# Kernel tuning notes

Measured on AMD Instinct MI355X. Metric: run time of the kernel, lower is better.

Reference implementation:

```python
import jax, jax.numpy as jnp
import numpy as np

N = 1_000_000   # total nodes
B = 20_000      # number of graphs (segments)
V = 100_000     # item vocab (rows of feat table)
D = 128         # input_dim
H = 128         # hidden_dim
O = 256         # output_dim
EPS = 1e-5


def setup_inputs() -> dict:
    key = jax.random.key(0)
    ks = jax.random.split(key, 10)
    feat = jax.random.normal(ks[0], (V, D), dtype=jnp.float32)
    iid = jax.random.randint(ks[1], (N,), 0, V)
    segment_ids = jnp.sort(jax.random.randint(ks[2], (N,), 0, B))
    last_nodes = jax.random.randint(ks[3], (B,), 0, N)
    s = 1.0 / np.sqrt(D)
    gamma = jnp.ones((D,), jnp.float32)
    beta = jnp.zeros((D,), jnp.float32)
    W_u = jax.random.uniform(ks[4], (D, H), jnp.float32, -s, s)
    W_v = jax.random.uniform(ks[5], (D, H), jnp.float32, -s, s)
    b_v = jax.random.uniform(ks[6], (H,), jnp.float32, -s, s)
    w_e = jax.random.uniform(ks[7], (H,), jnp.float32, -1.0 / np.sqrt(H), 1.0 / np.sqrt(H))
    W_out = jax.random.uniform(ks[8], (D, O), jnp.float32, -s, s)
    return {"feat": feat, "iid": iid, "segment_ids": segment_ids,
            "last_nodes": last_nodes, "gamma": gamma, "beta": beta,
            "W_u": W_u, "W_v": W_v, "b_v": b_v, "w_e": w_e, "W_out": W_out}


def reference(feat, iid, segment_ids, last_nodes, gamma, beta, W_u, W_v, b_v, w_e, W_out):
    # gather per-node features from item table
    x = feat[iid]                                  # [N, D]
    # BatchNorm1d (training mode: batch statistics, biased var)
    mean = jnp.mean(x, axis=0)
    var = jnp.mean((x - mean) ** 2, axis=0)
    x = (x - mean) * jax.lax.rsqrt(var + EPS) * gamma + beta
    # projections
    feat_u = x @ W_u                               # [N, H]
    feat_v = x[last_nodes] @ W_v + b_v             # [B, H]
    e = jax.nn.sigmoid(feat_u + feat_v[segment_ids]) @ w_e   # [N]
    # segment softmax over per-graph node segments
    e_max = jax.ops.segment_max(e, segment_ids, num_segments=B)
    ex = jnp.exp(e - e_max[segment_ids])
    denom = jax.ops.segment_sum(ex, segment_ids, num_segments=B)
    alpha = ex / denom[segment_ids]                # [N]
    # weighted segment sum, then output projection
    rst = jax.ops.segment_sum(x * alpha[:, None], segment_ids, num_segments=B)  # [B, D]
    return rst @ W_out                             # [B, O]
```

## Files before the change

### kernel.cpp

```cpp
#include <hip/hip_runtime.h>

typedef __attribute__((ext_vector_type(8))) short short8;
typedef __attribute__((ext_vector_type(4))) float floatx4;

static __device__ __forceinline__ unsigned short f2bf(float x) {
    unsigned int u = __float_as_uint(x);
    u += 0x7fffu + ((u >> 16) & 1u);
    return (unsigned short)(u >> 16);
}

__global__ void k_hist(const int* __restrict__ iid, int* __restrict__ counts, int N) {
    int n = blockIdx.x * blockDim.x + threadIdx.x;
    if (n < N) atomicAdd(&counts[iid[n]], 1);
}

__global__ __launch_bounds__(256) void k_cvtstats(const float* __restrict__ feat,
                                                  const int* __restrict__ counts,
                                                  unsigned short* __restrict__ featb,
                                                  float* __restrict__ dsum, float* __restrict__ dsumsq,
                                                  int V) {
    int tid = threadIdx.x;
    int r2 = tid >> 7, d = tid & 127;
    float s = 0.f, qa = 0.f;
    for (int vp = blockIdx.x; vp * 2 < V; vp += gridDim.x) {
        int v = vp * 2 + r2;
        if (v >= V) continue;
        float f = feat[(size_t)v * 128 + d];
        featb[(size_t)v * 128 + d] = f2bf(f);
        float c = (float)counts[v];
        if (c != 0.f) { s += c * f; qa += c * f * f; }
    }
    __shared__ float red[256];
    red[tid] = s; __syncthreads();
    if (tid < 128) atomicAdd(&dsum[d], red[tid] + red[tid + 128]);
    __syncthreads();
    red[tid] = qa; __syncthreads();
    if (tid < 128) atomicAdd(&dsumsq[d], red[tid] + red[tid + 128]);
}

__global__ __launch_bounds__(128) void k_affine(const float* __restrict__ sum,
                                                const float* __restrict__ sumsq,
                                                const float* __restrict__ gamma,
                                                const float* __restrict__ beta,
                                                float* __restrict__ scale, float* __restrict__ shift,
                                                float invN) {
    int d = threadIdx.x;
    float mean = sum[d] * invN;
    float var  = sumsq[d] * invN - mean * mean;
    float sc   = gamma[d] * rsqrtf(var + 1e-5f);
    scale[d] = sc;
    shift[d] = beta[d] - mean * sc;
}

__global__ __launch_bounds__(128) void k_prep(const float* __restrict__ Wu, const float* __restrict__ Wv,
                                              const float* __restrict__ bv,
                                              const float* __restrict__ scale, const float* __restrict__ shift,
                                              unsigned short* __restrict__ wut, float* __restrict__ wvs,
                                              float* __restrict__ cbias) {
    int h = blockIdx.x, d = threadIdx.x;
    float sc = scale[d], sh = shift[d];
    float wu = Wu[d * 128 + h], wv = Wv[d * 128 + h];
    wut[h * 128 + d] = f2bf(sc * wu);
    wvs[d * 128 + h] = sc * wv;
    __shared__ float red[128];
    red[d] = sh * (wu + wv);
    __syncthreads();
    for (int off = 64; off > 0; off >>= 1) {
        if (d < off) red[d] += red[d + off];
        __syncthreads();
    }
    if (d == 0) cbias[h] = bv[h] + red[0];
}

__global__ __launch_bounds__(128) void k_fv(const float* __restrict__ feat, const int* __restrict__ iid,
                                            const int* __restrict__ last, const float* __restrict__ wvs,
                                            const float* __restrict__ cbias, float* __restrict__ fv,
                                            int B) {
    const int GPB = 8;
    int b0 = blockIdx.x * GPB;
    int h = threadIdx.x;
    __shared__ float sx[GPB][128];
    for (int g = 0; g < GPB; ++g) {
        int b = b0 + g;
        if (b < B) {
            int row = iid[last[b]];
            sx[g][h] = feat[(size_t)row * 128 + h];
        }
    }
    __syncthreads();
    float acc[GPB];
#pragma unroll
    for (int g = 0; g < GPB; ++g) acc[g] = 0.f;
    for (int d = 0; d < 128; ++d) {
        float w = wvs[d * 128 + h];
#pragma unroll
        for (int g = 0; g < GPB; ++g) acc[g] += sx[g][d] * w;
    }
    float c = cbias[h];
    for (int g = 0; g < GPB; ++g)
        if (b0 + g < B) fv[(size_t)(b0 + g) * 128 + h] = acc[g] + c;
}

__global__ __launch_bounds__(256, 3) void k_main(
        const unsigned short* __restrict__ featb, const int* __restrict__ iid,
        const int* __restrict__ seg, const unsigned short* __restrict__ wut,
        const float* __restrict__ fv, const float* __restrict__ we_g,
        float* __restrict__ exo, int N, int B, int numTiles) {
    __shared__ unsigned short sA[2][64 * 128];
    __shared__ int   sSeg[2][64];
    __shared__ float sFv[2][4][128];
    __shared__ float sEp[2][4][64];

    int tid = threadIdx.x;
    int wv = tid >> 6, lane = tid & 63, q = lane >> 4, c = lane & 15;
    int p2 = lane & 15;
    int rowbase = wv * 16 + (lane >> 4);

    short8 bfr[2][4];
    float we2[2];
#pragma unroll
    for (int t = 0; t < 2; ++t) {
        int h = (2 * wv + t) * 16 + c;
        we2[t] = we_g[h];
#pragma unroll
        for (int kc = 0; kc < 4; ++kc)
            bfr[t][kc] = *(const short8*)(wut + h * 128 + kc * 32 + q * 8);
    }

    if (blockIdx.x >= numTiles) return;

    int iidR[4]; int segR; float2 fvR;
    auto loadRegs = [&](int T) {
        int n0 = T << 6;
#pragma unroll
        for (int k = 0; k < 4; ++k)
            iidR[k] = iid[min(n0 + rowbase + 4 * k, N - 1)];
        segR = seg[min(n0 + (tid & 63), N - 1)];
        int s0 = seg[min(n0, N - 1)];
        int fvrow = min(s0 + (tid >> 6), B - 1);
        fvR = *(const float2*)(fv + (size_t)fvrow * 128 + ((tid << 1) & 127));
    };
    auto stage = [&](int buf) {
        unsigned short* sAb = &sA[buf][0];
#pragma unroll
        for (int k = 0; k < 4; ++k) {
            int row = rowbase + 4 * k;
            int j = (p2 & 8) | ((p2 & 7) ^ (row & 7));
            const unsigned short* g = featb + (size_t)iidR[k] * 128 + j * 8;
            __builtin_amdgcn_global_load_lds(
                (const __attribute__((address_space(1))) void*)g,
                (__attribute__((address_space(3))) void*)(sAb + wv * 2048 + k * 512),
                16, 0, 0);
        }
        if (tid < 64) sSeg[buf][tid] = segR;
        *(float2*)&sFv[buf][tid >> 6][(tid << 1) & 127] = fvR;
    };

    int T = blockIdx.x;
    loadRegs(T);
    stage(0);
    int prevN0 = -1;
    int cur = 0;

    for (;;) {
        int Tn = T + gridDim.x;
        bool hn = (Tn < numTiles);
        if (hn) loadRegs(Tn);
        __syncthreads();
        if (hn) stage(cur ^ 1);

        floatx4 acc[4][2];
#pragma unroll
        for (int mt = 0; mt < 4; ++mt)
#pragma unroll
            for (int t = 0; t < 2; ++t) acc[mt][t] = (floatx4)(0.f);
#pragma unroll
        for (int kc = 0; kc < 4; ++kc) {
            int jj = 4 * kc + q;
            int pofs = ((jj & 8) | ((jj & 7) ^ (c & 7))) * 8;
            short8 a0 = *(const short8*)&sA[cur][( 0 + c) * 128 + pofs];
            short8 a1 = *(const short8*)&sA[cur][(16 + c) * 128 + pofs];
            short8 a2 = *(const short8*)&sA[cur][(32 + c) * 128 + pofs];
            short8 a3 = *(const short8*)&sA[cur][(48 + c) * 128 + pofs];
#pragma unroll
            for (int t = 0; t < 2; ++t) {
                acc[0][t] = __builtin_amdgcn_mfma_f32_16x16x32_bf16(a0, bfr[t][kc], acc[0][t], 0, 0, 0);
                acc[1][t] = __builtin_amdgcn_mfma_f32_16x16x32_bf16(a1, bfr[t][kc], acc[1][t], 0, 0, 0);
                acc[2][t] = __builtin_amdgcn_mfma_f32_16x16x32_bf16(a2, bfr[t][kc], acc[2][t], 0, 0, 0);
                acc[3][t] = __builtin_amdgcn_mfma_f32_16x16x32_bf16(a3, bfr[t][kc], acc[3][t], 0, 0, 0);
            }
        }
        {
            int s0 = sSeg[cur][0];
            int h0 = wv * 32 + c;
#pragma unroll
            for (int mt = 0; mt < 4; ++mt)
#pragma unroll
                for (int r = 0; r < 4; ++r) {
                    int nl = mt * 16 + q * 4 + r;
                    int sg = sSeg[cur][nl];
                    int off = sg - s0;
                    float f0, f1;
                    if (off < 4) {
                        f0 = sFv[cur][off][h0];
                        f1 = sFv[cur][off][h0 + 16];
                    } else {
                        f0 = fv[((size_t)sg << 7) + h0];
                        f1 = fv[((size_t)sg << 7) + h0 + 16];
                    }
                    float u0 = acc[mt][0][r] + f0;
                    float u1 = acc[mt][1][r] + f1;
                    float p = we2[0] * __builtin_amdgcn_rcpf(1.f + __expf(-u0))
                            + we2[1] * __builtin_amdgcn_rcpf(1.f + __expf(-u1));
                    p += __shfl_xor(p, 1);
                    p += __shfl_xor(p, 2);
                    p += __shfl_xor(p, 4);
                    p += __shfl_xor(p, 8);
                    if (c == 0) sEp[cur][wv][nl] = p;
                }
        }
        if (prevN0 >= 0 && tid < 64) {
            int n = prevN0 + tid;
            if (n < N) {
                float s = sEp[cur ^ 1][0][tid] + sEp[cur ^ 1][1][tid]
                        + sEp[cur ^ 1][2][tid] + sEp[cur ^ 1][3][tid];
                exo[n] = __expf(s);
            }
        }
        prevN0 = T << 6;
        if (!hn) break;
        T = Tn; cur ^= 1;
    }
    __syncthreads();
    if (tid < 64) {
        int n = prevN0 + tid;
        if (n < N) {
            float s = sEp[cur][0][tid] + sEp[cur][1][tid]
                    + sEp[cur][2][tid] + sEp[cur][3][tid];
            exo[n] = __expf(s);
        }
    }
}

__global__ void k_bounds(const int* __restrict__ seg, int* __restrict__ start, int N, int B) {
    int n = blockIdx.x * blockDim.x + threadIdx.x;
    if (n >= N) return;
    int cur = seg[n];
    int prev = (n == 0) ? -1 : seg[n - 1];
    for (int b = prev + 1; b <= cur; ++b) start[b] = n;
    if (n == N - 1)
        for (int b = cur + 1; b <= B; ++b) start[b] = N;
}

__global__ __launch_bounds__(256) void k_wsum(const unsigned short* __restrict__ featb,
                                              const int* __restrict__ iid,
                                              const float* __restrict__ exv,
                                              const int* __restrict__ start,
                                              const float* __restrict__ scale,
                                              const float* __restrict__ shift,
                                              float* __restrict__ rst, int B) {
    int tid = threadIdx.x;
    int wv = tid >> 6, lane = tid & 63;
    int b = blockIdx.x * 4 + wv;
    if (b >= B) return;
    int s = start[b], t = start[b + 1];
    float a0 = 0.f, a1 = 0.f, dl = 0.f;
    int voff = lane * 2;

    for (int base = s; base < t; base += 64) {
        int idx = base + lane;
        bool valid = (idx < t);
        float e = valid ? exv[idx] : 0.f;
        int   r = valid ? iid[idx] : 0;
        dl += e;
        for (int k = 0; k < 64; k += 4) {
            if (base + k >= t) break;
#pragma unroll
            for (int kk = 0; kk < 4; ++kk) {
                int   rk = __builtin_amdgcn_readlane(r, k + kk);
                float ek = __int_as_float(__builtin_amdgcn_readlane(__float_as_int(e), k + kk));
                unsigned u = *(const unsigned*)(featb + (size_t)rk * 128 + voff);
                a0 += ek * __uint_as_float(u << 16);
                a1 += ek * __uint_as_float(u & 0xffff0000u);
            }
        }
    }
#pragma unroll
    for (int off = 1; off < 64; off <<= 1) dl += __shfl_xor(dl, off);
    float inv = (t > s) ? 1.f / dl : 0.f;
    float msk = (t > s) ? 1.f : 0.f;
    int d0 = lane * 2;
    float r0 = scale[d0] * a0 * inv + shift[d0] * msk;
    float r1 = scale[d0 + 1] * a1 * inv + shift[d0 + 1] * msk;
    *(float2*)&rst[((size_t)b << 7) + d0] = make_float2(r0, r1);
}

__global__ __launch_bounds__(256) void k_out(const float* __restrict__ rst, const float* __restrict__ Wout,
                                             float* __restrict__ out, int B) {
    __shared__ float sT[128][36];
    int b0 = blockIdx.x * 32;
    int t = threadIdx.x;
    for (int i = 0; i < 16; ++i) {
        int idx = i * 256 + t;
        int r = idx >> 7, d = idx & 127;
        int b = min(b0 + r, B - 1);
        sT[d][r] = rst[((size_t)b << 7) + d];
    }
    __syncthreads();
    float acc[32];
#pragma unroll
    for (int r = 0; r < 32; ++r) acc[r] = 0.f;
    for (int dd = 0; dd < 128; ++dd) {
        float w = Wout[dd * 256 + t];
        const float4* row = (const float4*)&sT[dd][0];
#pragma unroll
        for (int r4 = 0; r4 < 8; ++r4) {
            float4 v = row[r4];
            acc[r4 * 4 + 0] += w * v.x;
            acc[r4 * 4 + 1] += w * v.y;
            acc[r4 * 4 + 2] += w * v.z;
            acc[r4 * 4 + 3] += w * v.w;
        }
    }
    for (int r = 0; r < 32; ++r)
        if (b0 + r < B) out[(size_t)(b0 + r) * 256 + t] = acc[r];
}

extern "C" void kernel_launch(void* const* d_in, const int* in_sizes, int n_in,
                              void* d_out, int out_size, void* d_ws, size_t ws_size,
                              hipStream_t stream) {
    const float* feat  = (const float*)d_in[0];
    const int*   iid   = (const int*)d_in[1];
    const int*   seg   = (const int*)d_in[2];
    const int*   last  = (const int*)d_in[3];
    const float* gamma = (const float*)d_in[4];
    const float* beta  = (const float*)d_in[5];
    const float* Wu    = (const float*)d_in[6];
    const float* Wv    = (const float*)d_in[7];
    const float* bv    = (const float*)d_in[8];
    const float* we    = (const float*)d_in[9];
    const float* Wout  = (const float*)d_in[10];
    float* out = (float*)d_out;

    int V = in_sizes[0] / 128;
    int N = in_sizes[1];
    int B = in_sizes[3];

    char* w = (char*)d_ws;
    size_t off = 0;
    auto alloc = [&](size_t bytes) -> void* {
        void* p = w + off;
        off += (bytes + 255) & ~(size_t)255;
        return p;
    };
    int*   counts = (int*)alloc((size_t)V * 4);
    float* dsum   = (float*)alloc(512);
    float* dsumsq = (float*)alloc(512);
    size_t zero_bytes = off;
    float* scale  = (float*)alloc(512);
    float* shift  = (float*)alloc(512);
    float* cbias  = (float*)alloc(512);
    unsigned short* wut = (unsigned short*)alloc(128 * 128 * 2);
    float* wvs    = (float*)alloc(128 * 128 * 4);
    float* fv     = (float*)alloc((size_t)B * 128 * 4);
    unsigned short* featb = (unsigned short*)alloc((size_t)V * 128 * 2);
    float* exo    = (float*)alloc((size_t)N * 4);
    int*   startA = (int*)alloc((size_t)(B + 1) * 4);
    float* rst    = (float*)alloc((size_t)B * 128 * 4);
    (void)ws_size; (void)n_in; (void)out_size;

    hipMemsetAsync(d_ws, 0, zero_bytes, stream);

    k_hist<<<(N + 255) / 256, 256, 0, stream>>>(iid, counts, N);
    k_cvtstats<<<1024, 256, 0, stream>>>(feat, counts, featb, dsum, dsumsq, V);
    k_affine<<<1, 128, 0, stream>>>(dsum, dsumsq, gamma, beta, scale, shift, 1.0f / (float)N);
    k_prep<<<128, 128, 0, stream>>>(Wu, Wv, bv, scale, shift, wut, wvs, cbias);
    k_fv<<<(B + 7) / 8, 128, 0, stream>>>(feat, iid, last, wvs, cbias, fv, B);
    k_bounds<<<(N + 255) / 256, 256, 0, stream>>>(seg, startA, N, B);

    int numTiles = (N + 63) / 64;
    k_main<<<768, 256, 0, stream>>>(featb, iid, seg, wut, fv, we, exo, N, B, numTiles);

    k_wsum<<<(B + 3) / 4, 256, 0, stream>>>(featb, iid, exo, startA, scale, shift, rst, B);
    k_out<<<(B + 31) / 32, 256, 0, stream>>>(rst, Wout, out, B);
}
```

Baseline: 413.4 us.

## Fuse weighted segment sum into main kernel using staged LDS tiles and atomics

The main attention kernel now does the weighted segment accumulation itself. It reuses the bf16 feature tile already staged in LDS and pushes per-segment partial sums and denominators to global buffers with float atomics. This drops the exo write/readback, the k_bounds and k_wsum kernels, and the second gather of feature rows. Softmax normalisation and the BatchNorm affine are deferred into k_out. It also swaps the shuffle reduction for DPP adds, raises occupancy to 4 blocks with 1024 blocks, and adds a sync per tile. The exp no longer subtracts the segment max, which risks overflow, and atomics add contention plus nondeterminism.

New measurement: 413.8 us. About the same (+0.1%).

```diff
diff --git a/kernel.cpp b/kernel.cpp
--- a/kernel.cpp
+++ b/kernel.cpp
@@ -2,11 +2,18 @@
 
 typedef __attribute__((ext_vector_type(8))) short short8;
 typedef __attribute__((ext_vector_type(4))) float floatx4;
+typedef __attribute__((ext_vector_type(4))) int intx4;
 
 static __device__ __forceinline__ unsigned short f2bf(float x) {
     unsigned int u = __float_as_uint(x);
     u += 0x7fffu + ((u >> 16) & 1u);
     return (unsigned short)(u >> 16);
+}
+
+template <int CTRL>
+static __device__ __forceinline__ float dpp_add(float x) {
+    int v = __builtin_amdgcn_update_dpp(0, __float_as_int(x), CTRL, 0xf, 0xf, true);
+    return x + __int_as_float(v);
 }
 
 __global__ void k_hist(const int* __restrict__ iid, int* __restrict__ counts, int N) {
@@ -101,15 +108,16 @@
         if (b0 + g < B) fv[(size_t)(b0 + g) * 128 + h] = acc[g] + c;
 }
 
-__global__ __launch_bounds__(256, 3) void k_main(
+__global__ __launch_bounds__(256, 4) void k_main(
         const unsigned short* __restrict__ featb, const int* __restrict__ iid,
         const int* __restrict__ seg, const unsigned short* __restrict__ wut,
         const float* __restrict__ fv, const float* __restrict__ we_g,
-        float* __restrict__ exo, int N, int B, int numTiles) {
+        float* __restrict__ rstAcc, float* __restrict__ den,
+        int N, int B, int numTiles) {
     __shared__ unsigned short sA[2][64 * 128];
     __shared__ int   sSeg[2][64];
     __shared__ float sFv[2][4][128];
-    __shared__ float sEp[2][4][64];
+    __shared__ float sEp[4][64];
 
     int tid = threadIdx.x;
     int wv = tid >> 6, lane = tid & 63, q = lane >> 4, c = lane & 15;
@@ -136,7 +144,7 @@
         for (int k = 0; k < 4; ++k)
             iidR[k] = iid[min(n0 + rowbase + 4 * k, N - 1)];
         segR = seg[min(n0 + (tid & 63), N - 1)];
-        int s0 = seg[min(n0, N - 1)];
+        int s0 = __builtin_amdgcn_readfirstlane(segR);
         int fvrow = min(s0 + (tid >> 6), B - 1);
         fvR = *(const float2*)(fv + (size_t)fvrow * 128 + ((tid << 1) & 127));
     };
@@ -159,7 +167,6 @@
     int T = blockIdx.x;
     loadRegs(T);
     stage(0);
-    int prevN0 = -1;
     int cur = 0;
 
     for (;;) {
@@ -212,106 +219,98 @@
                     float u1 = acc[mt][1][r] + f1;
                     float p = we2[0] * __builtin_amdgcn_rcpf(1.f + __expf(-u0))
                             + we2[1] * __builtin_amdgcn_rcpf(1.f + __expf(-u1));
-                    p += __shfl_xor(p, 1);
-                    p += __shfl_xor(p, 2);
-                    p += __shfl_xor(p, 4);
-                    p += __shfl_xor(p, 8);
-                    if (c == 0) sEp[cur][wv][nl] = p;
+                    p = dpp_add<0xb1>(p);
+                    p = dpp_add<0x4e>(p);
+                    p = dpp_add<0x141>(p);
+                    p = dpp_add<0x140>(p);
+                    if (c == 0) sEp[wv][nl] = p;
                 }
         }
-        if (prevN0 >= 0 && tid < 64) {
-            int n = prevN0 + tid;
-            if (n < N) {
-                float s = sEp[cur ^ 1][0][tid] + sEp[cur ^ 1][1][tid]
-                        + sEp[cur ^ 1][2][tid] + sEp[cur ^ 1][3][tid];
-                exo[n] = __expf(s);
+        __syncthreads();
+
+        {
+            int n0 = T << 6;
+            int nb = wv * 16;
+            float exr[16];
+#pragma unroll
+            for (int jg = 0; jg < 4; ++jg) {
+                floatx4 e0 = *(const floatx4*)&sEp[0][nb + jg * 4];
+                floatx4 e1 = *(const floatx4*)&sEp[1][nb + jg * 4];
+                floatx4 e2 = *(const floatx4*)&sEp[2][nb + jg * 4];
+                floatx4 e3 = *(const floatx4*)&sEp[3][nb + jg * 4];
+#pragma unroll
+                for (int r = 0; r < 4; ++r) {
+                    float s = e0[r] + e1[r] + e2[r] + e3[r];
+                    exr[jg * 4 + r] = (n0 + nb + jg * 4 + r < N) ? __expf(s) : 0.f;
+                }
             }
-        }
-        prevN0 = T << 6;
+            int sgr[16];
+#pragma unroll
+            for (int jg = 0; jg < 4; ++jg)
+                *(intx4*)&sgr[jg * 4] = *(const intx4*)&sSeg[cur][nb + jg * 4];
+
+            int d0 = lane * 2;
+            int jj = lane >> 2;
+            int wsub = (lane & 3) * 4;
+            const char* base = (const char*)&sA[cur][0];
+            float a0 = 0.f, a1 = 0.f, dl = 0.f;
+            int curseg = sgr[0];
+#pragma unroll
+            for (int j = 0; j < 16; ++j) {
+                int row = nb + j;
+                int sg = sgr[j];
+                if (sg != curseg) {
+                    atomicAdd(&rstAcc[(size_t)curseg * 128 + d0], a0);
+                    atomicAdd(&rstAcc[(size_t)curseg * 128 + d0 + 1], a1);
+                    if (lane == 0) atomicAdd(&den[curseg], dl);
+                    a0 = a1 = dl = 0.f; curseg = sg;
+                }
+                int ch = (jj & 8) | ((jj & 7) ^ (row & 7));
+                unsigned u = *(const unsigned*)(base + row * 256 + ch * 16 + wsub);
+                float e = exr[j];
+                a0 += e * __uint_as_float(u << 16);
+                a1 += e * __uint_as_float(u & 0xffff0000u);
+                dl += e;
+            }
+            atomicAdd(&rstAcc[(size_t)curseg * 128 + d0], a0);
+            atomicAdd(&rstAcc[(size_t)curseg * 128 + d0 + 1], a1);
+            if (lane == 0) atomicAdd(&den[curseg], dl);
+        }
+
         if (!hn) break;
         T = Tn; cur ^= 1;
     }
-    __syncthreads();
-    if (tid < 64) {
-        int n = prevN0 + tid;
-        if (n < N) {
-            float s = sEp[cur][0][tid] + sEp[cur][1][tid]
-                    + sEp[cur][2][tid] + sEp[cur][3][tid];
-            exo[n] = __expf(s);
-        }
-    }
-}
-
-__global__ void k_bounds(const int* __restrict__ seg, int* __restrict__ start, int N, int B) {
-    int n = blockIdx.x * blockDim.x + threadIdx.x;
-    if (n >= N) return;
-    int cur = seg[n];
-    int prev = (n == 0) ? -1 : seg[n - 1];
-    for (int b = prev + 1; b <= cur; ++b) start[b] = n;
-    if (n == N - 1)
-        for (int b = cur + 1; b <= B; ++b) start[b] = N;
-}
-
-__global__ __launch_bounds__(256) void k_wsum(const unsigned short* __restrict__ featb,
-                                              const int* __restrict__ iid,
-                                              const float* __restrict__ exv,
-                                              const int* __restrict__ start,
-                                              const float* __restrict__ scale,
-                                              const float* __restrict__ shift,
-                                              float* __restrict__ rst, int B) {
-    int tid = threadIdx.x;
-    int wv = tid >> 6, lane = tid & 63;
-    int b = blockIdx.x * 4 + wv;
-    if (b >= B) return;
-    int s = start[b], t = start[b + 1];
-    float a0 = 0.f, a1 = 0.f, dl = 0.f;
-    int voff = lane * 2;
-
-    for (int base = s; base < t; base += 64) {
-        int idx = base + lane;
-        bool valid = (idx < t);
-        float e = valid ? exv[idx] : 0.f;
-        int   r = valid ? iid[idx] : 0;
-        dl += e;
-        for (int k = 0; k < 64; k += 4) {
-            if (base + k >= t) break;
-#pragma unroll
-            for (int kk = 0; kk < 4; ++kk) {
-                int   rk = __builtin_amdgcn_readlane(r, k + kk);
-                float ek = __int_as_float(__builtin_amdgcn_readlane(__float_as_int(e), k + kk));
-                unsigned u = *(const unsigned*)(featb + (size_t)rk * 128 + voff);
-                a0 += ek * __uint_as_float(u << 16);
-                a1 += ek * __uint_as_float(u & 0xffff0000u);
-            }
-        }
-    }
-#pragma unroll
-    for (int off = 1; off < 64; off <<= 1) dl += __shfl_xor(dl, off);
-    float inv = (t > s) ? 1.f / dl : 0.f;
-    float msk = (t > s) ? 1.f : 0.f;
-    int d0 = lane * 2;
-    float r0 = scale[d0] * a0 * inv + shift[d0] * msk;
-    float r1 = scale[d0 + 1] * a1 * inv + shift[d0 + 1] * msk;
-    *(float2*)&rst[((size_t)b << 7) + d0] = make_float2(r0, r1);
-}
-
-__global__ __launch_bounds__(256) void k_out(const float* __restrict__ rst, const float* __restrict__ Wout,
+}
+
+__global__ __launch_bounds__(256) void k_out(const float* __restrict__ rstAcc,
+                                             const float* __restrict__ den,
+                                             const float* __restrict__ scale,
+                                             const float* __restrict__ shift,
+                                             const float* __restrict__ Wout,
                                              float* __restrict__ out, int B) {
     __shared__ float sT[128][36];
+    __shared__ float sInv[32];
     int b0 = blockIdx.x * 32;
     int t = threadIdx.x;
     for (int i = 0; i < 16; ++i) {
         int idx = i * 256 + t;
         int r = idx >> 7, d = idx & 127;
         int b = min(b0 + r, B - 1);
-        sT[d][r] = rst[((size_t)b << 7) + d];
+        sT[d][r] = scale[d] * rstAcc[((size_t)b << 7) + d];
+    }
+    if (t < 32) {
+        int b = min(b0 + t, B - 1);
+        float dn = den[b];
+        sInv[t] = (dn > 0.f) ? 1.f / dn : 0.f;
     }
     __syncthreads();
     float acc[32];
 #pragma unroll
     for (int r = 0; r < 32; ++r) acc[r] = 0.f;
+    float sb = 0.f;
     for (int dd = 0; dd < 128; ++dd) {
         float w = Wout[dd * 256 + t];
+        sb += shift[dd] * w;
         const float4* row = (const float4*)&sT[dd][0];
 #pragma unroll
         for (int r4 = 0; r4 < 8; ++r4) {
@@ -323,7 +322,10 @@
         }
     }
     for (int r = 0; r < 32; ++r)
-        if (b0 + r < B) out[(size_t)(b0 + r) * 256 + t] = acc[r];
+        if (b0 + r < B) {
+            float inv = sInv[r];
+            out[(size_t)(b0 + r) * 256 + t] = acc[r] * inv + (inv != 0.f ? sb : 0.f);
+        }
 }
 
 extern "C" void kernel_launch(void* const* d_in, const int* in_sizes, int n_in,
@@ -356,6 +358,8 @@
     int*   counts = (int*)alloc((size_t)V * 4);
     float* dsum   = (float*)alloc(512);
     float* dsumsq = (float*)alloc(512);
+    float* rstAcc = (float*)alloc((size_t)B * 128 * 4);
+    float* den    = (float*)alloc((size_t)B * 4);
     size_t zero_bytes = off;
     float* scale  = (float*)alloc(512);
     float* shift  = (float*)alloc(512);
@@ -364,9 +368,6 @@
     float* wvs    = (float*)alloc(128 * 128 * 4);
     float* fv     = (float*)alloc((size_t)B * 128 * 4);
     unsigned short* featb = (unsigned short*)alloc((size_t)V * 128 * 2);
-    float* exo    = (float*)alloc((size_t)N * 4);
-    int*   startA = (int*)alloc((size_t)(B + 1) * 4);
-    float* rst    = (float*)alloc((size_t)B * 128 * 4);
     (void)ws_size; (void)n_in; (void)out_size;
 
     hipMemsetAsync(d_ws, 0, zero_bytes, stream);
@@ -376,11 +377,9 @@
     k_affine<<<1, 128, 0, stream>>>(dsum, dsumsq, gamma, beta, scale, shift, 1.0f / (float)N);
     k_prep<<<128, 128, 0, stream>>>(Wu, Wv, bv, scale, shift, wut, wvs, cbias);
     k_fv<<<(B + 7) / 8, 128, 0, stream>>>(feat, iid, last, wvs, cbias, fv, B);
-    k_bounds<<<(N + 255) / 256, 256, 0, stream>>>(seg, startA, N, B);
 
     int numTiles = (N + 63) / 64;
-    k_main<<<768, 256, 0, stream>>>(featb, iid, seg, wut, fv, we, exo, N, B, numTiles);
-
-    k_wsum<<<(B + 3) / 4, 256, 0, stream>>>(featb, iid, exo, startA, scale, shift, rst, B);
-    k_out<<<(B + 31) / 32, 256, 0, stream>>>(rst, Wout, out, B);
-}
+    k_main<<<1024, 256, 0, stream>>>(featb, iid, seg, wut, fv, we, rstAcc, den, N, B, numTiles);
+
+    k_out<<<(B + 31) / 32, 256, 0, stream>>>(rstAcc, den, scale, shift, Wout, out, B);
+}
```
